# Performance work log

Measured on AMD Instinct MI355X. Metric: run time of the kernel, lower is better.

## Reference

```python
import jax, jax.numpy as jnp
import numpy as np

NUM_CLASSES = 80
CONF_THRE = 0.2
NMS_THRE = 0.45
MAX_DET = 300   # fixed cap replacing torch's variable-length NMS output (padded + keep mask)
IMG = 640.0


def setup_inputs() -> dict:
    key = jax.random.key(0)
    k1, k2 = jax.random.split(key)
    pred = jax.random.uniform(k1, (32, 8400, 85), dtype=jnp.float32)
    # scale cx,cy,w,h to pixel range so IoU/NMS geometry is realistic
    pred = pred.at[..., :4].multiply(IMG)
    zone = jax.random.uniform(k2, (8, 2), dtype=jnp.float32) * IMG
    return {"prediction": pred, "zone": zone}


def _pairwise_iou(b):
    # b: [B, K, 4] in x1y1x2y2
    area = jnp.clip(b[..., 2] - b[..., 0], 0.0) * jnp.clip(b[..., 3] - b[..., 1], 0.0)
    lt = jnp.maximum(b[:, :, None, :2], b[:, None, :, :2])
    rb = jnp.minimum(b[:, :, None, 2:], b[:, None, :, 2:])
    wh = jnp.clip(rb - lt, 0.0)
    inter = wh[..., 0] * wh[..., 1]
    return inter / (area[:, :, None] + area[:, None, :] - inter + 1e-9)


def _postprocess(prediction):
    # decode cx,cy,w,h -> x1,y1,x2,y2
    xy = prediction[..., :2]
    wh = prediction[..., 2:4]
    boxes = jnp.concatenate([xy - wh * 0.5, xy + wh * 0.5], axis=-1)  # [B,N,4]
    obj = prediction[..., 4]                                           # [B,N]
    cls = prediction[..., 5:5 + NUM_CLASSES]
    class_conf = jnp.max(cls, axis=-1)                                 # [B,N]
    class_pred = jnp.argmax(cls, axis=-1)                              # [B,N]

    # confidence mask (obj * class_conf >= thre); invalid -> -inf so top_k drops them
    nms_score = obj * class_conf
    nms_score = jnp.where(nms_score >= CONF_THRE, nms_score, -jnp.inf)

    s, idx = jax.lax.top_k(nms_score, MAX_DET)                         # [B,K]
    b = jnp.take_along_axis(boxes, idx[..., None], axis=1)             # [B,K,4]

    # class-agnostic greedy NMS on score-sorted boxes (matches torchvision.ops.nms)
    iou = _pairwise_iou(b)                                             # [B,K,K]
    keep = jnp.isfinite(s)                                             # valid (passed conf) entries
    ar = jnp.arange(MAX_DET)
    def body(i, keep):
        sup = keep[:, i][:, None] & (iou[:, i, :] > NMS_THRE) & (ar > i)
        return keep & jnp.logical_not(sup)
    keep = jax.lax.fori_loop(0, MAX_DET, body, keep)

    obj_s = jnp.take_along_axis(obj, idx, axis=1)
    conf_s = jnp.take_along_axis(class_conf, idx, axis=1)
    cls_s = jnp.take_along_axis(class_pred, idx, axis=1).astype(jnp.int32)
    # extract_boxes_scores_and_classes: score = max over columns [obj, class_conf]
    scores = jnp.maximum(obj_s, conf_s)
    return b, scores, cls_s, keep


def _points_inside_zone(px, py, zone):
    # px, py: [B,K]; zone: [Z,2]. Ray-casting parity test (faithful to torch version).
    zr = jnp.roll(zone, shift=1, axis=0)
    xi, yi = zone[:, 0], zone[:, 1]
    xj, yj = zr[:, 0], zr[:, 1]
    pyb = py[..., None]  # [B,K,1] vs [Z]
    pxb = px[..., None]
    gyi = yi > pyb
    gyj = yj > pyb
    gx = (xj - xi) * (pyb - yi) / (yj - yi) + xi
    inter = (gyi != gyj) & (gx > pxb)
    return (jnp.sum(inter.astype(jnp.int32), axis=-1) % 2) > 0


def reference(prediction, zone):
    b, scores, classes, keep = _postprocess(prediction)
    cx = (b[..., 0] + b[..., 2]) * 0.5
    cy = (b[..., 1] + b[..., 3]) * 0.5
    in_zone = _points_inside_zone(cx, cy, zone) & keep
    centers_yx = jnp.stack([cy, cx], axis=-1)                          # [B,K,2]
    boxes_yxyx = jnp.stack([b[..., 1], b[..., 0], b[..., 3], b[..., 2]], axis=-1)
    return boxes_yxyx, in_zone, scores, classes, centers_yx, keep
```

## Files before the change

kernel.cpp:

```cpp
#include <hip/hip_runtime.h>
#include <stdint.h>

typedef unsigned long long ull;

#define NA 8400
#define NB 32
#define KTOP 300
#define NC 80
#define CH 33
#define WS_STRIDE 33600
#define OFF_SEL   0
#define OFF_KEEP  2400
#define OFF_MASK  2560

#define O1 38400
#define O2 48000
#define O3 57600
#define O4 67200
#define O5 86400

__global__ __launch_bounds__(256) void score_kernel(const float* __restrict__ pred,
                                                    uint32_t* __restrict__ keys) {
    __shared__ float sP[128 * 85];
    const int blk = blockIdx.x;
    const float4* g4 = (const float4*)(pred + (size_t)blk * 128 * 85);
    float4* l4 = (float4*)sP;
    for (int i = threadIdx.x; i < (128 * 85 / 4); i += 256) l4[i] = g4[i];
    __syncthreads();
    const int t = threadIdx.x;
    if (t < 128) {
        const float* p = sP + t * 85;
        float obj = p[4];
        float b0 = p[5], b1 = p[6], b2 = p[7], b3 = p[8];
        #pragma unroll
        for (int c = 4; c < NC; c += 4) {
            b0 = fmaxf(b0, p[5 + c]);
            b1 = fmaxf(b1, p[6 + c]);
            b2 = fmaxf(b2, p[7 + c]);
            b3 = fmaxf(b3, p[8 + c]);
        }
        float best = fmaxf(fmaxf(b0, b1), fmaxf(b2, b3));
        float sc = obj * best;
        uint32_t u = (sc >= 0.2f) ? (__float_as_uint(sc) | 0x80000000u) : 0x007FFFFFu;
        keys[(size_t)blk * 128 + t] = u;
    }
}

__global__ __launch_bounds__(256) void select_kernel(const uint32_t* keys, uint8_t* ws) {
    __shared__ uint32_t sKeys[8448];
    __shared__ ull sSel[KTOP];
    __shared__ ull sSorted[KTOP];
    __shared__ uint32_t sH4[1024];
    __shared__ uint32_t sScanA[256];
    __shared__ uint32_t sScanB[256];
    __shared__ uint32_t sBc[2];
    __shared__ int sCnt;

    const int b = blockIdx.x;
    const int t = threadIdx.x;
    const int wv = t >> 6;

    for (int e = t; e < NA; e += 256) sKeys[e] = keys[(size_t)b * NA + e];
    for (int e = NA + t; e < 8448; e += 256) sKeys[e] = 0u;
    if (t == 0) sCnt = 0;
    __syncthreads();

    uint32_t prefix = 0, r = KTOP;
    const int beg = t * CH;
    const int end = (beg + CH < NA) ? beg + CH : NA;
    for (int round = 0; round < 4; ++round) {
        const int shift = 24 - 8 * round;
        for (int idx = t; idx < 1024; idx += 256) sH4[idx] = 0u;
        __syncthreads();
        const uint32_t pmask = (round == 0) ? 0u : (0xFFFFFFFFu << (shift + 8));
        for (int e = beg; e < end; ++e) {
            uint32_t k = sKeys[e];
            if ((k & pmask) == (prefix & pmask))
                atomicAdd(&sH4[(wv << 8) + ((k >> shift) & 0xFFu)], 1u);
        }
        __syncthreads();
        sScanA[t] = sH4[t] + sH4[256 + t] + sH4[512 + t] + sH4[768 + t];
        __syncthreads();
        uint32_t* src = sScanA;
        uint32_t* dst = sScanB;
        for (int off = 1; off < 256; off <<= 1) {
            uint32_t v = src[t];
            if (t + off < 256) v += src[t + off];
            dst[t] = v;
            __syncthreads();
            uint32_t* tmp = src; src = dst; dst = tmp;
        }
        uint32_t S = src[t];
        uint32_t above = (t < 255) ? src[t + 1] : 0;
        if (above < r && S >= r) {
            sBc[0] = prefix | ((uint32_t)t << shift);
            sBc[1] = r - above;
        }
        __syncthreads();
        prefix = sBc[0]; r = sBc[1];
        __syncthreads();
    }
    const uint32_t kth = prefix;
    const uint32_t rem = r;
    const uint32_t cntgt = KTOP - rem;

    {
        uint32_t eqc = 0;
        for (int e = beg; e < end; ++e) {
            uint32_t k = sKeys[e];
            if (k > kth) {
                int p = atomicAdd(&sCnt, 1);
                sSel[p] = ((ull)k << 32) | (ull)(0xFFFFFFFFu - (uint32_t)e);
            } else if (k == kth) eqc++;
        }
        sScanA[t] = eqc;
        __syncthreads();
        uint32_t* src = sScanA;
        uint32_t* dst = sScanB;
        for (int off = 1; off < 256; off <<= 1) {
            uint32_t v = src[t];
            if (t >= off) v += src[t - off];
            dst[t] = v;
            __syncthreads();
            uint32_t* tmp = src; src = dst; dst = tmp;
        }
        uint32_t off0 = (t > 0) ? src[t - 1] : 0;
        for (int e = beg; e < end; ++e) {
            uint32_t k = sKeys[e];
            if (k == kth) {
                if (off0 < rem)
                    sSel[cntgt + off0] = ((ull)k << 32) | (ull)(0xFFFFFFFFu - (uint32_t)e);
                off0++;
            }
        }
        __syncthreads();
    }

    ull my0 = sSel[t];
    ull my1 = (t < KTOP - 256) ? sSel[256 + t] : 0ull;
    int r0 = 0, r1 = 0;
    for (int j = 0; j < KTOP; ++j) {
        ull v = sSel[j];
        r0 += (v > my0) ? 1 : 0;
        r1 += (v > my1) ? 1 : 0;
    }
    sSorted[r0] = my0;
    if (t < KTOP - 256) sSorted[r1] = my1;
    __syncthreads();

    ull* selW = (ull*)(ws + (size_t)b * WS_STRIDE + OFF_SEL);
    ull* keepW = (ull*)(ws + (size_t)b * WS_STRIDE + OFF_KEEP);
    bool f = ((uint32_t)(sSorted[t] >> 32)) > 0x007FFFFFu;
    ull m = __ballot(f);
    if ((t & 63) == 0) keepW[t >> 6] = m;
    if (t < 64) {
        bool f2 = (t < KTOP - 256) && (((uint32_t)(sSorted[256 + t] >> 32)) > 0x007FFFFFu);
        ull m2 = __ballot(f2);
        if (t == 0) keepW[4] = m2;
    }
    selW[t] = sSorted[t];
    if (t < KTOP - 256) selW[256 + t] = sSorted[256 + t];
}

__global__ __launch_bounds__(256) void prep_kernel(const float* __restrict__ pred,
                                                   uint8_t* ws,
                                                   float* __restrict__ out) {
    #pragma clang fp contract(off)
    __shared__ float sB0[KTOP], sB1[KTOP], sB2[KTOP], sB3[KTOP];
    const int role = blockIdx.x;
    const int b = blockIdx.y;
    const int t = threadIdx.x;
    const ull* sel = (const ull*)(ws + (size_t)b * WS_STRIDE + OFF_SEL);

    if (role < 5) {
        for (int i = t; i < KTOP; i += 256) {
            uint32_t a = 0xFFFFFFFFu - (uint32_t)sel[i];
            const float* p = pred + ((size_t)b * NA + a) * 85;
            float x = p[0], y = p[1], w = p[2], h = p[3];
            float hw = w * 0.5f, hh = h * 0.5f;
            sB0[i] = x - hw; sB1[i] = y - hh; sB2[i] = x + hw; sB3[i] = y + hh;
        }
        __syncthreads();
        ull* mask = (ull*)(ws + (size_t)b * WS_STRIDE + OFF_MASK);
        const int j0 = role * 64;
        int jmax = j0 + 64; if (jmax > KTOP) jmax = KTOP;
        for (int i = t; i < KTOP; i += 256) {
            float x1 = sB0[i], y1 = sB1[i], x2 = sB2[i], y2 = sB3[i];
            float ai = fmaxf(x2 - x1, 0.0f) * fmaxf(y2 - y1, 0.0f);
            ull bits = 0ull;
            int jbeg = (j0 > i + 1) ? j0 : (i + 1);
            for (int j = jbeg; j < jmax; ++j) {
                float bx1 = sB0[j], by1 = sB1[j], bx2 = sB2[j], by2 = sB3[j];
                float aj = fmaxf(bx2 - bx1, 0.0f) * fmaxf(by2 - by1, 0.0f);
                float iw = fminf(x2, bx2) - fmaxf(x1, bx1); iw = fmaxf(iw, 0.0f);
                float ih = fminf(y2, by2) - fmaxf(y1, by1); ih = fmaxf(ih, 0.0f);
                float inter = iw * ih;
                float den = ai + aj;
                den = den - inter;
                den = den + 1e-9f;
                float iou = inter / den;
                if (iou > 0.45f) bits |= (1ull << (j - j0));
            }
            mask[i * 5 + role] = bits;
        }
    } else {
        const size_t bo = (size_t)b * KTOP;
        for (int i = t; i < KTOP; i += 256) {
            uint32_t a = 0xFFFFFFFFu - (uint32_t)sel[i];
            const float* p = pred + ((size_t)b * NA + a) * 85;
            float x = p[0], y = p[1], w = p[2], h = p[3], obj = p[4];
            float best = p[5]; int bc = 0;
            for (int c = 1; c < NC; ++c) {
                float v = p[5 + c];
                if (v > best) { best = v; bc = c; }
            }
            float hw = w * 0.5f, hh = h * 0.5f;
            float x1 = x - hw, y1 = y - hh, x2 = x + hw, y2 = y + hh;
            out[(bo + i) * 4 + 0] = y1;
            out[(bo + i) * 4 + 1] = x1;
            out[(bo + i) * 4 + 2] = y2;
            out[(bo + i) * 4 + 3] = x2;
            out[O4 + (bo + i) * 2 + 0] = (y1 + y2) * 0.5f;
            out[O4 + (bo + i) * 2 + 1] = (x1 + x2) * 0.5f;
            out[O2 + bo + i] = fmaxf(obj, best);
            out[O3 + bo + i] = (float)bc;
        }
    }
}

__global__ __launch_bounds__(64) void finish_kernel(const float* __restrict__ zone,
                                                    const uint8_t* ws,
                                                    float* __restrict__ out) {
    #pragma clang fp contract(off)
    __shared__ float sZone[16];
    const int b = blockIdx.x;
    const int L = threadIdx.x;
    const ull* mask = (const ull*)(ws + (size_t)b * WS_STRIDE + OFF_MASK);
    const ull* keepI = (const ull*)(ws + (size_t)b * WS_STRIDE + OFF_KEEP);
    if (L < 16) sZone[L] = zone[L];

    ull rm[5][5];
    #pragma unroll
    for (int w = 0; w < 5; ++w) {
        int i = w * 64 + L;
        #pragma unroll
        for (int ww = 0; ww < 5; ++ww)
            rm[w][ww] = (i < KTOP) ? mask[i * 5 + ww] : 0ull;
    }
    ull kw[5];
    #pragma unroll
    for (int w = 0; w < 5; ++w) kw[w] = keepI[w];
    __syncthreads();

    #pragma unroll
    for (int w = 0; w < 5; ++w) {
        ull cur = kw[w];
        while (cur) {
            int ib = __builtin_ctzll(cur);
            ull m0 = __shfl(rm[w][0], ib);
            ull m1 = __shfl(rm[w][1], ib);
            ull m2 = __shfl(rm[w][2], ib);
            ull m3 = __shfl(rm[w][3], ib);
            ull m4 = __shfl(rm[w][4], ib);
            kw[0] &= ~m0; kw[1] &= ~m1; kw[2] &= ~m2; kw[3] &= ~m3; kw[4] &= ~m4;
            ull done = (ib == 63) ? 0ull : (~0ull << (ib + 1));
            cur = kw[w] & done;
        }
    }

    const size_t bo = (size_t)b * KTOP;
    #pragma unroll
    for (int h = 0; h < 5; ++h) {
        int i = h * 64 + L;
        if (i < KTOP) {
            int kp = (int)((kw[h] >> L) & 1ull);
            float cy = out[O4 + (bo + i) * 2 + 0];
            float cx = out[O4 + (bo + i) * 2 + 1];
            int cnt = 0;
            #pragma unroll
            for (int e = 0; e < 8; ++e) {
                float xi = sZone[2 * e], yi = sZone[2 * e + 1];
                int ep = (e + 7) & 7;
                float xj = sZone[2 * ep], yj = sZone[2 * ep + 1];
                bool gyi = yi > cy, gyj = yj > cy;
                if (gyi != gyj) {
                    float gx = (xj - xi) * (cy - yi) / (yj - yi) + xi;
                    if (gx > cx) cnt++;
                }
            }
            int inz = (((cnt & 1) != 0) && kp) ? 1 : 0;
            out[O1 + bo + i] = (float)inz;
            out[O5 + bo + i] = (float)kp;
        }
    }
}

extern "C" void kernel_launch(void* const* d_in, const int* in_sizes, int n_in,
                              void* d_out, int out_size, void* d_ws, size_t ws_size,
                              hipStream_t stream) {
    const float* pred = (const float*)d_in[0];
    const float* zone = (const float*)d_in[1];
    float* out = (float*)d_out;
    uint32_t* keys = (uint32_t*)d_ws;
    uint8_t* ws = (uint8_t*)d_ws;

    score_kernel<<<(NB * NA) / 128, 256, 0, stream>>>(pred, keys);
    select_kernel<<<NB, 256, 0, stream>>>(keys, ws);
    prep_kernel<<<dim3(6, NB), 256, 0, stream>>>(pred, ws, out);
    finish_kernel<<<NB, 64, 0, stream>>>(zone, ws, out);
}
```

Measured before the change: 204.2 us.

## Fuse argmax into score pass, aggregate histogram atomics per wave, merge NMS stages

The score kernel now also computes the class argmax and writes compact per-anchor box and metadata records. The select kernel can then gather the top-300 boxes and write the box, score, class and center outputs directly, with no scattered re-reads of the 85-float rows. The radix-select histogram switches from per-thread atomics to wave-aggregated ballot/shuffle atomics, and the block scans use wave shuffles instead of shared-memory ping-pong with many barriers. The IoU mask build moves into the finish kernel and uses shared memory, which drops one kernel launch and the global mask round trip. The cost is extra workspace writes for the compacted records, and a serial loop over distinct bins inside the histogram ballot.

```diff
diff --git a/kernel.cpp b/kernel.cpp
--- a/kernel.cpp
+++ b/kernel.cpp
@@ -8,10 +8,12 @@
 #define KTOP 300
 #define NC 80
 #define CH 33
+
 #define WS_STRIDE 33600
-#define OFF_SEL   0
-#define OFF_KEEP  2400
-#define OFF_MASK  2560
+#define OFF_KEEP  0
+#define OFF_BOX   64
+#define XYWH_OFF  1075200
+#define META_OFF  5376000
 
 #define O1 38400
 #define O2 48000
@@ -19,45 +21,60 @@
 #define O4 67200
 #define O5 86400
 
-__global__ __launch_bounds__(256) void score_kernel(const float* __restrict__ pred,
-                                                    uint32_t* __restrict__ keys) {
+__global__ __launch_bounds__(128) void score_kernel(const float* __restrict__ pred,
+                                                    uint32_t* __restrict__ keys,
+                                                    float4* __restrict__ xywh4,
+                                                    float4* __restrict__ meta4) {
     __shared__ float sP[128 * 85];
     const int blk = blockIdx.x;
+    const int t = threadIdx.x;
     const float4* g4 = (const float4*)(pred + (size_t)blk * 128 * 85);
     float4* l4 = (float4*)sP;
-    for (int i = threadIdx.x; i < (128 * 85 / 4); i += 256) l4[i] = g4[i];
-    __syncthreads();
-    const int t = threadIdx.x;
-    if (t < 128) {
-        const float* p = sP + t * 85;
-        float obj = p[4];
-        float b0 = p[5], b1 = p[6], b2 = p[7], b3 = p[8];
-        #pragma unroll
-        for (int c = 4; c < NC; c += 4) {
-            b0 = fmaxf(b0, p[5 + c]);
-            b1 = fmaxf(b1, p[6 + c]);
-            b2 = fmaxf(b2, p[7 + c]);
-            b3 = fmaxf(b3, p[8 + c]);
-        }
-        float best = fmaxf(fmaxf(b0, b1), fmaxf(b2, b3));
-        float sc = obj * best;
-        uint32_t u = (sc >= 0.2f) ? (__float_as_uint(sc) | 0x80000000u) : 0x007FFFFFu;
-        keys[(size_t)blk * 128 + t] = u;
-    }
+    for (int i = t; i < (128 * 85 / 4); i += 128) l4[i] = g4[i];
+    __syncthreads();
+    const float* p = sP + t * 85;
+    float x = p[0], y = p[1], w = p[2], h = p[3], obj = p[4];
+    float b0 = p[5], b1 = p[6], b2 = p[7], b3 = p[8];
+    int i0 = 0, i1 = 1, i2 = 2, i3 = 3;
+    #pragma unroll
+    for (int c = 4; c < NC; c += 4) {
+        float v0 = p[5 + c], v1 = p[6 + c], v2 = p[7 + c], v3 = p[8 + c];
+        if (v0 > b0) { b0 = v0; i0 = c; }
+        if (v1 > b1) { b1 = v1; i1 = c + 1; }
+        if (v2 > b2) { b2 = v2; i2 = c + 2; }
+        if (v3 > b3) { b3 = v3; i3 = c + 3; }
+    }
+    float best = fmaxf(fmaxf(b0, b1), fmaxf(b2, b3));
+    int bi = 0x7FFFFFFF;
+    if (b3 == best) bi = i3;
+    if (b2 == best && i2 < bi) bi = i2;
+    if (b1 == best && i1 < bi) bi = i1;
+    if (b0 == best && i0 < bi) bi = i0;
+    float sc = obj * best;
+    uint32_t u = (sc >= 0.2f) ? (__float_as_uint(sc) | 0x80000000u) : 0x007FFFFFu;
+    const size_t gi = (size_t)blk * 128 + t;
+    keys[gi] = u;
+    xywh4[gi] = make_float4(x, y, w, h);
+    meta4[gi] = make_float4(obj, best, (float)bi, 0.0f);
 }
 
-__global__ __launch_bounds__(256) void select_kernel(const uint32_t* keys, uint8_t* ws) {
+__global__ __launch_bounds__(256) void select_kernel(const uint32_t* __restrict__ keys,
+                                                     const float4* __restrict__ xywh4,
+                                                     const float4* __restrict__ meta4,
+                                                     uint8_t* ws,
+                                                     float* __restrict__ out) {
+    #pragma clang fp contract(off)
     __shared__ uint32_t sKeys[8448];
     __shared__ ull sSel[KTOP];
     __shared__ ull sSorted[KTOP];
-    __shared__ uint32_t sH4[1024];
-    __shared__ uint32_t sScanA[256];
-    __shared__ uint32_t sScanB[256];
+    __shared__ uint32_t sHist[256];
+    __shared__ uint32_t sWs[8];
     __shared__ uint32_t sBc[2];
     __shared__ int sCnt;
 
     const int b = blockIdx.x;
     const int t = threadIdx.x;
+    const unsigned lane = t & 63;
     const int wv = t >> 6;
 
     for (int e = t; e < NA; e += 256) sKeys[e] = keys[(size_t)b * NA + e];
@@ -66,33 +83,47 @@
     __syncthreads();
 
     uint32_t prefix = 0, r = KTOP;
-    const int beg = t * CH;
-    const int end = (beg + CH < NA) ? beg + CH : NA;
     for (int round = 0; round < 4; ++round) {
         const int shift = 24 - 8 * round;
-        for (int idx = t; idx < 1024; idx += 256) sH4[idx] = 0u;
+        sHist[t] = 0u;
         __syncthreads();
         const uint32_t pmask = (round == 0) ? 0u : (0xFFFFFFFFu << (shift + 8));
-        for (int e = beg; e < end; ++e) {
-            uint32_t k = sKeys[e];
-            if ((k & pmask) == (prefix & pmask))
-                atomicAdd(&sH4[(wv << 8) + ((k >> shift) & 0xFFu)], 1u);
-        }
-        __syncthreads();
-        sScanA[t] = sH4[t] + sH4[256 + t] + sH4[512 + t] + sH4[768 + t];
-        __syncthreads();
-        uint32_t* src = sScanA;
-        uint32_t* dst = sScanB;
-        for (int off = 1; off < 256; off <<= 1) {
-            uint32_t v = src[t];
-            if (t + off < 256) v += src[t + off];
-            dst[t] = v;
-            __syncthreads();
-            uint32_t* tmp = src; src = dst; dst = tmp;
-        }
-        uint32_t S = src[t];
-        uint32_t above = (t < 255) ? src[t + 1] : 0;
-        if (above < r && S >= r) {
+        const uint32_t pval = prefix & pmask;
+        for (int s = 0; s < CH; ++s) {
+            int e = t * CH + s;
+            bool act = (e < NA);
+            uint32_t k = act ? sKeys[e] : 0u;
+            act = act && ((k & pmask) == pval);
+            uint32_t bin = (k >> shift) & 0xFFu;
+            ull todo = __ballot(act);
+            while (todo) {
+                int leader = __builtin_ctzll(todo);
+                uint32_t lbin = __shfl((int)bin, leader);
+                ull eq = __ballot(act && (bin == lbin));
+                if (lane == (unsigned)leader)
+                    atomicAdd(&sHist[lbin], (uint32_t)__popcll(eq));
+                todo &= ~eq;
+            }
+        }
+        __syncthreads();
+        uint32_t h = sHist[t];
+        uint32_t val = h;
+        #pragma unroll
+        for (int d = 1; d < 64; d <<= 1) {
+            uint32_t v = __shfl_up(val, d);
+            if (lane >= (unsigned)d) val += v;
+        }
+        if (lane == 63) sWs[wv] = val;
+        __syncthreads();
+        if (t == 0) {
+            uint32_t a = sWs[0], b2 = sWs[1], c = sWs[2];
+            sWs[4] = 0; sWs[5] = a; sWs[6] = a + b2; sWs[7] = a + b2 + c;
+        }
+        __syncthreads();
+        uint32_t P = val + sWs[4 + wv];
+        uint32_t Total = sWs[7] + sWs[3];
+        uint32_t above = Total - P;
+        if (above < r && above + h >= r) {
             sBc[0] = prefix | ((uint32_t)t << shift);
             sBc[1] = r - above;
         }
@@ -106,31 +137,39 @@
 
     {
         uint32_t eqc = 0;
-        for (int e = beg; e < end; ++e) {
-            uint32_t k = sKeys[e];
-            if (k > kth) {
-                int p = atomicAdd(&sCnt, 1);
-                sSel[p] = ((ull)k << 32) | (ull)(0xFFFFFFFFu - (uint32_t)e);
-            } else if (k == kth) eqc++;
-        }
-        sScanA[t] = eqc;
-        __syncthreads();
-        uint32_t* src = sScanA;
-        uint32_t* dst = sScanB;
-        for (int off = 1; off < 256; off <<= 1) {
-            uint32_t v = src[t];
-            if (t >= off) v += src[t - off];
-            dst[t] = v;
-            __syncthreads();
-            uint32_t* tmp = src; src = dst; dst = tmp;
-        }
-        uint32_t off0 = (t > 0) ? src[t - 1] : 0;
-        for (int e = beg; e < end; ++e) {
-            uint32_t k = sKeys[e];
-            if (k == kth) {
-                if (off0 < rem)
-                    sSel[cntgt + off0] = ((ull)k << 32) | (ull)(0xFFFFFFFFu - (uint32_t)e);
-                off0++;
+        for (int s = 0; s < CH; ++s) {
+            int e = t * CH + s;
+            if (e < NA) {
+                uint32_t k = sKeys[e];
+                if (k > kth) {
+                    int p = atomicAdd(&sCnt, 1);
+                    sSel[p] = ((ull)k << 32) | (ull)(0xFFFFFFFFu - (uint32_t)e);
+                } else if (k == kth) eqc++;
+            }
+        }
+        uint32_t val = eqc;
+        #pragma unroll
+        for (int d = 1; d < 64; d <<= 1) {
+            uint32_t v = __shfl_up(val, d);
+            if (lane >= (unsigned)d) val += v;
+        }
+        if (lane == 63) sWs[wv] = val;
+        __syncthreads();
+        if (t == 0) {
+            uint32_t a = sWs[0], b2 = sWs[1], c = sWs[2];
+            sWs[4] = 0; sWs[5] = a; sWs[6] = a + b2; sWs[7] = a + b2 + c;
+        }
+        __syncthreads();
+        uint32_t off0 = val - eqc + sWs[4 + wv];
+        for (int s = 0; s < CH; ++s) {
+            int e = t * CH + s;
+            if (e < NA) {
+                uint32_t k = sKeys[e];
+                if (k == kth) {
+                    if (off0 < rem)
+                        sSel[cntgt + off0] = ((ull)k << 32) | (ull)(0xFFFFFFFFu - (uint32_t)e);
+                    off0++;
+                }
             }
         }
         __syncthreads();
@@ -148,150 +187,135 @@
     if (t < KTOP - 256) sSorted[r1] = my1;
     __syncthreads();
 
-    ull* selW = (ull*)(ws + (size_t)b * WS_STRIDE + OFF_SEL);
     ull* keepW = (ull*)(ws + (size_t)b * WS_STRIDE + OFF_KEEP);
-    bool f = ((uint32_t)(sSorted[t] >> 32)) > 0x007FFFFFu;
-    ull m = __ballot(f);
-    if ((t & 63) == 0) keepW[t >> 6] = m;
-    if (t < 64) {
-        bool f2 = (t < KTOP - 256) && (((uint32_t)(sSorted[256 + t] >> 32)) > 0x007FFFFFu);
-        ull m2 = __ballot(f2);
-        if (t == 0) keepW[4] = m2;
-    }
-    selW[t] = sSorted[t];
-    if (t < KTOP - 256) selW[256 + t] = sSorted[256 + t];
+    {
+        bool f = ((uint32_t)(sSorted[t] >> 32)) > 0x007FFFFFu;
+        ull m = __ballot(f);
+        if (lane == 0) keepW[wv] = m;
+        if (t < 64) {
+            bool f2 = (t < KTOP - 256) && (((uint32_t)(sSorted[256 + t] >> 32)) > 0x007FFFFFu);
+            ull m2 = __ballot(f2);
+            if (t == 0) keepW[4] = m2;
+        }
+    }
+
+    float4* wsBox = (float4*)(ws + (size_t)b * WS_STRIDE + OFF_BOX);
+    const size_t bo = (size_t)b * KTOP;
+    for (int i = t; i < KTOP; i += 256) {
+        ull s = sSorted[i];
+        uint32_t a = 0xFFFFFFFFu - (uint32_t)(s & 0xFFFFFFFFull);
+        size_t g = (size_t)b * NA + a;
+        float4 xw = xywh4[g];
+        float4 mt = meta4[g];
+        float hw = xw.z * 0.5f, hh = xw.w * 0.5f;
+        float x1 = xw.x - hw, y1 = xw.y - hh, x2 = xw.x + hw, y2 = xw.y + hh;
+        wsBox[i] = make_float4(x1, y1, x2, y2);
+        ((float4*)out)[bo + i] = make_float4(y1, x1, y2, x2);
+        ((float2*)(out + O4))[bo + i] = make_float2((y1 + y2) * 0.5f,
+                                                    (x1 + x2) * 0.5f);
+        out[O2 + bo + i] = fmaxf(mt.x, mt.y);
+        out[O3 + bo + i] = mt.z;
+    }
 }
 
-__global__ __launch_bounds__(256) void prep_kernel(const float* __restrict__ pred,
-                                                   uint8_t* ws,
-                                                   float* __restrict__ out) {
+__global__ __launch_bounds__(256) void finish_kernel(const float* __restrict__ zone,
+                                                     const uint8_t* __restrict__ ws,
+                                                     float* __restrict__ out) {
     #pragma clang fp contract(off)
-    __shared__ float sB0[KTOP], sB1[KTOP], sB2[KTOP], sB3[KTOP];
-    const int role = blockIdx.x;
-    const int b = blockIdx.y;
-    const int t = threadIdx.x;
-    const ull* sel = (const ull*)(ws + (size_t)b * WS_STRIDE + OFF_SEL);
-
-    if (role < 5) {
-        for (int i = t; i < KTOP; i += 256) {
-            uint32_t a = 0xFFFFFFFFu - (uint32_t)sel[i];
-            const float* p = pred + ((size_t)b * NA + a) * 85;
-            float x = p[0], y = p[1], w = p[2], h = p[3];
-            float hw = w * 0.5f, hh = h * 0.5f;
-            sB0[i] = x - hw; sB1[i] = y - hh; sB2[i] = x + hw; sB3[i] = y + hh;
-        }
-        __syncthreads();
-        ull* mask = (ull*)(ws + (size_t)b * WS_STRIDE + OFF_MASK);
-        const int j0 = role * 64;
-        int jmax = j0 + 64; if (jmax > KTOP) jmax = KTOP;
-        for (int i = t; i < KTOP; i += 256) {
-            float x1 = sB0[i], y1 = sB1[i], x2 = sB2[i], y2 = sB3[i];
-            float ai = fmaxf(x2 - x1, 0.0f) * fmaxf(y2 - y1, 0.0f);
-            ull bits = 0ull;
-            int jbeg = (j0 > i + 1) ? j0 : (i + 1);
-            for (int j = jbeg; j < jmax; ++j) {
-                float bx1 = sB0[j], by1 = sB1[j], bx2 = sB2[j], by2 = sB3[j];
-                float aj = fmaxf(bx2 - bx1, 0.0f) * fmaxf(by2 - by1, 0.0f);
-                float iw = fminf(x2, bx2) - fmaxf(x1, bx1); iw = fmaxf(iw, 0.0f);
-                float ih = fminf(y2, by2) - fmaxf(y1, by1); ih = fmaxf(ih, 0.0f);
-                float inter = iw * ih;
-                float den = ai + aj;
-                den = den - inter;
-                den = den + 1e-9f;
-                float iou = inter / den;
-                if (iou > 0.45f) bits |= (1ull << (j - j0));
-            }
-            mask[i * 5 + role] = bits;
-        }
-    } else {
-        const size_t bo = (size_t)b * KTOP;
-        for (int i = t; i < KTOP; i += 256) {
-            uint32_t a = 0xFFFFFFFFu - (uint32_t)sel[i];
-            const float* p = pred + ((size_t)b * NA + a) * 85;
-            float x = p[0], y = p[1], w = p[2], h = p[3], obj = p[4];
-            float best = p[5]; int bc = 0;
-            for (int c = 1; c < NC; ++c) {
-                float v = p[5 + c];
-                if (v > best) { best = v; bc = c; }
-            }
-            float hw = w * 0.5f, hh = h * 0.5f;
-            float x1 = x - hw, y1 = y - hh, x2 = x + hw, y2 = y + hh;
-            out[(bo + i) * 4 + 0] = y1;
-            out[(bo + i) * 4 + 1] = x1;
-            out[(bo + i) * 4 + 2] = y2;
-            out[(bo + i) * 4 + 3] = x2;
-            out[O4 + (bo + i) * 2 + 0] = (y1 + y2) * 0.5f;
-            out[O4 + (bo + i) * 2 + 1] = (x1 + x2) * 0.5f;
-            out[O2 + bo + i] = fmaxf(obj, best);
-            out[O3 + bo + i] = (float)bc;
-        }
-    }
-}
-
-__global__ __launch_bounds__(64) void finish_kernel(const float* __restrict__ zone,
-                                                    const uint8_t* ws,
-                                                    float* __restrict__ out) {
-    #pragma clang fp contract(off)
+    __shared__ float4 sBox[KTOP];
+    __shared__ ull sMask[5 * KTOP];
+    __shared__ ull sKeepOut[5];
     __shared__ float sZone[16];
     const int b = blockIdx.x;
-    const int L = threadIdx.x;
-    const ull* mask = (const ull*)(ws + (size_t)b * WS_STRIDE + OFF_MASK);
-    const ull* keepI = (const ull*)(ws + (size_t)b * WS_STRIDE + OFF_KEEP);
-    if (L < 16) sZone[L] = zone[L];
-
-    ull rm[5][5];
-    #pragma unroll
-    for (int w = 0; w < 5; ++w) {
-        int i = w * 64 + L;
-        #pragma unroll
-        for (int ww = 0; ww < 5; ++ww)
-            rm[w][ww] = (i < KTOP) ? mask[i * 5 + ww] : 0ull;
-    }
-    ull kw[5];
-    #pragma unroll
-    for (int w = 0; w < 5; ++w) kw[w] = keepI[w];
-    __syncthreads();
-
-    #pragma unroll
-    for (int w = 0; w < 5; ++w) {
-        ull cur = kw[w];
-        while (cur) {
-            int ib = __builtin_ctzll(cur);
-            ull m0 = __shfl(rm[w][0], ib);
-            ull m1 = __shfl(rm[w][1], ib);
-            ull m2 = __shfl(rm[w][2], ib);
-            ull m3 = __shfl(rm[w][3], ib);
-            ull m4 = __shfl(rm[w][4], ib);
-            kw[0] &= ~m0; kw[1] &= ~m1; kw[2] &= ~m2; kw[3] &= ~m3; kw[4] &= ~m4;
-            ull done = (ib == 63) ? 0ull : (~0ull << (ib + 1));
-            cur = kw[w] & done;
-        }
-    }
+    const int t = threadIdx.x;
+    const float4* wsBox = (const float4*)(ws + (size_t)b * WS_STRIDE + OFF_BOX);
+    const ull* keepW = (const ull*)(ws + (size_t)b * WS_STRIDE + OFF_KEEP);
+
+    if (t < 16) sZone[t] = zone[t];
+    for (int i = t; i < KTOP; i += 256) sBox[i] = wsBox[i];
+    __syncthreads();
+
+    for (int item = t; item < 5 * KTOP; item += 256) {
+        int role = item / KTOP;
+        int i = item - role * KTOP;
+        float4 B = sBox[i];
+        float x1 = B.x, y1 = B.y, x2 = B.z, y2 = B.w;
+        float ai = fmaxf(x2 - x1, 0.0f) * fmaxf(y2 - y1, 0.0f);
+        ull bits = 0ull;
+        int j0 = role * 64;
+        int jmax = j0 + 64; if (jmax > KTOP) jmax = KTOP;
+        int jbeg = (j0 > i + 1) ? j0 : (i + 1);
+        for (int j = jbeg; j < jmax; ++j) {
+            float4 C = sBox[j];
+            float aj = fmaxf(C.z - C.x, 0.0f) * fmaxf(C.w - C.y, 0.0f);
+            float iw = fminf(x2, C.z) - fmaxf(x1, C.x); iw = fmaxf(iw, 0.0f);
+            float ih = fminf(y2, C.w) - fmaxf(y1, C.y); ih = fmaxf(ih, 0.0f);
+            float inter = iw * ih;
+            float den = ai + aj;
+            den = den - inter;
+            den = den + 1e-9f;
+            float iou = inter / den;
+            if (iou > 0.45f) bits |= (1ull << (j - j0));
+        }
+        sMask[item] = bits;
+    }
+    __syncthreads();
+
+    if (t < 64) {
+        ull rm[5][5];
+        #pragma unroll
+        for (int w = 0; w < 5; ++w) {
+            int i = w * 64 + t;
+            #pragma unroll
+            for (int ww = 0; ww < 5; ++ww)
+                rm[w][ww] = (i < KTOP) ? sMask[ww * KTOP + i] : 0ull;
+        }
+        ull kw[5];
+        #pragma unroll
+        for (int w = 0; w < 5; ++w) kw[w] = keepW[w];
+        #pragma unroll
+        for (int w = 0; w < 5; ++w) {
+            ull cur = kw[w];
+            while (cur) {
+                int ib = __builtin_ctzll(cur);
+                ull m0 = __shfl(rm[w][0], ib);
+                ull m1 = __shfl(rm[w][1], ib);
+                ull m2 = __shfl(rm[w][2], ib);
+                ull m3 = __shfl(rm[w][3], ib);
+                ull m4 = __shfl(rm[w][4], ib);
+                kw[0] &= ~m0; kw[1] &= ~m1; kw[2] &= ~m2; kw[3] &= ~m3; kw[4] &= ~m4;
+                ull done = (ib == 63) ? 0ull : (~0ull << (ib + 1));
+                cur = kw[w] & done;
+            }
+        }
+        if (t == 0) {
+            #pragma unroll
+            for (int w = 0; w < 5; ++w) sKeepOut[w] = kw[w];
+        }
+    }
+    __syncthreads();
 
     const size_t bo = (size_t)b * KTOP;
-    #pragma unroll
-    for (int h = 0; h < 5; ++h) {
-        int i = h * 64 + L;
-        if (i < KTOP) {
-            int kp = (int)((kw[h] >> L) & 1ull);
-            float cy = out[O4 + (bo + i) * 2 + 0];
-            float cx = out[O4 + (bo + i) * 2 + 1];
-            int cnt = 0;
-            #pragma unroll
-            for (int e = 0; e < 8; ++e) {
-                float xi = sZone[2 * e], yi = sZone[2 * e + 1];
-                int ep = (e + 7) & 7;
-                float xj = sZone[2 * ep], yj = sZone[2 * ep + 1];
-                bool gyi = yi > cy, gyj = yj > cy;
-                if (gyi != gyj) {
-                    float gx = (xj - xi) * (cy - yi) / (yj - yi) + xi;
-                    if (gx > cx) cnt++;
-                }
-            }
-            int inz = (((cnt & 1) != 0) && kp) ? 1 : 0;
-            out[O1 + bo + i] = (float)inz;
-            out[O5 + bo + i] = (float)kp;
-        }
+    for (int i = t; i < KTOP; i += 256) {
+        int kp = (int)((sKeepOut[i >> 6] >> (i & 63)) & 1ull);
+        float4 B = sBox[i];
+        float cy = (B.y + B.w) * 0.5f;
+        float cx = (B.x + B.z) * 0.5f;
+        int cnt = 0;
+        #pragma unroll
+        for (int e = 0; e < 8; ++e) {
+            float xi = sZone[2 * e], yi = sZone[2 * e + 1];
+            int ep = (e + 7) & 7;
+            float xj = sZone[2 * ep], yj = sZone[2 * ep + 1];
+            bool gyi = yi > cy, gyj = yj > cy;
+            if (gyi != gyj) {
+                float gx = (xj - xi) * (cy - yi) / (yj - yi) + xi;
+                if (gx > cx) cnt++;
+            }
+        }
+        int inz = (((cnt & 1) != 0) && kp) ? 1 : 0;
+        out[O1 + bo + i] = (float)inz;
+        out[O5 + bo + i] = (float)kp;
     }
 }
 
@@ -301,11 +325,12 @@
     const float* pred = (const float*)d_in[0];
     const float* zone = (const float*)d_in[1];
     float* out = (float*)d_out;
-    uint32_t* keys = (uint32_t*)d_ws;
     uint8_t* ws = (uint8_t*)d_ws;
-
-    score_kernel<<<(NB * NA) / 128, 256, 0, stream>>>(pred, keys);
-    select_kernel<<<NB, 256, 0, stream>>>(keys, ws);
-    prep_kernel<<<dim3(6, NB), 256, 0, stream>>>(pred, ws, out);
-    finish_kernel<<<NB, 64, 0, stream>>>(zone, ws, out);
+    uint32_t* keys = (uint32_t*)ws;
+    float4* xywh4 = (float4*)(ws + XYWH_OFF);
+    float4* meta4 = (float4*)(ws + META_OFF);
+
+    score_kernel<<<(NB * NA) / 128, 128, 0, stream>>>(pred, keys, xywh4, meta4);
+    select_kernel<<<NB, 256, 0, stream>>>(keys, xywh4, meta4, ws, out);
+    finish_kernel<<<NB, 256, 0, stream>>>(zone, ws, out);
 }
```

Measured after the change: 330.5 us. 1.62x slower.
